# Kernel tuning notes

Measured on AMD Instinct MI355X. Metric: run time of the kernel, lower is better.

The kernel has to match this reference:

```python
import jax, jax.numpy as jnp
import numpy as np

V, N, K, D = 2, 100000, 8, 128
TAU = 1.0
LOG_2PI = float(np.log(2.0 * np.pi))


def setup_inputs() -> dict:
    key = jax.random.key(0)
    k1, k2, k3 = jax.random.split(key, 3)
    z = jax.random.normal(k1, (V, N, D), dtype=jnp.float32)
    phi = jnp.ones((V, K), dtype=jnp.float32) / K
    mu = jax.random.normal(k2, (V, K, D), dtype=jnp.float32)
    # sigma: identity (as in torch init) plus a small symmetric PSD perturbation
    a = 0.05 * jax.random.normal(k3, (V, K, D, D), dtype=jnp.float32)
    sigma = jnp.eye(D, dtype=jnp.float32) + jnp.einsum('vkde,vkfe->vkdf', a, a)
    return {"z": z, "phi": phi, "mu": mu, "sigma": sigma}


def _compute_energy(z, phi, mu, sigma):
    # z: [N, D]; phi: [K]; mu: [K, D]; sigma: [K, D, D]
    eps_eye = 1e-6 * jnp.eye(D, dtype=z.dtype)
    sigma_stable = sigma + eps_eye  # [K, D, D]
    inv_sigma = jnp.linalg.inv(sigma_stable)
    det_sigma = jnp.clip(jnp.linalg.det(sigma_stable), 1e-6, None)  # [K]
    diff = z[:, None, :] - mu[None, :, :]  # [N, K, D]
    maha = jnp.einsum('nkd,kde,nke->nk', diff, inv_sigma, diff)  # [N, K]
    log_pi = jax.nn.log_softmax(phi)  # [K]
    log_prob = (-0.5 * maha
                - 0.5 * D * LOG_2PI
                - 0.5 * jnp.log(det_sigma)[None, :]
                + log_pi[None, :])  # [N, K]
    energy = -jax.nn.logsumexp(log_prob, axis=1)  # [N]
    penalty = jnp.sum(1.0 / (jnp.diagonal(sigma_stable, axis1=-2, axis2=-1) + 1e-12))
    return energy, penalty


def reference(z, phi, mu, sigma):
    # vmap over views; energies_v: [V, N]
    energies_v, penalties = jax.vmap(_compute_energy)(z, phi, mu, sigma)
    energies = energies_v.T  # [N, V]
    total_energies = jnp.sum(energies)
    total_penalty = jnp.sum(penalties)
    weights = jax.nn.softmax(-energies / TAU, axis=1)  # [N, V]
    return energies, weights, total_energies, total_penalty
```

## Files before the change

### kernel.cpp

```cpp
#include <hip/hip_runtime.h>
#include <math.h>

#define V 2
#define NN 100000
#define KK 8
#define DD 128
#define TILE_N 128
#define SL 132
#define LOG2PI 1.8378770664093454f
#define LOG_1EM6 -13.815510557964274f

#define WLO_B 524288
#define BV_B  1048576
#define C_B   1056768

#define OUT_W_OFF (NN*V)
#define OUT_TE (2*NN*V)
#define OUT_TP (2*NN*V + 1)

typedef __attribute__((ext_vector_type(8))) short bf16x8;
typedef __attribute__((ext_vector_type(4))) float f32x4;

__device__ __forceinline__ unsigned short f2bf_rtn(float f) {
    unsigned u = __builtin_bit_cast(unsigned, f);
    unsigned r = u + 0x7FFFu + ((u >> 16) & 1u);
    return (unsigned short)(r >> 16);
}
__device__ __forceinline__ float bf2f(unsigned short h) {
    unsigned u = ((unsigned)h) << 16;
    return __builtin_bit_cast(float, u);
}

__global__ void zero_kernel(float* out) {
    int t = threadIdx.x;
    if (t < 2) out[OUT_TE + t] = 0.0f;
}

__global__ __launch_bounds__(256) void prep_kernel(const float* __restrict__ phi,
                                                   const float* __restrict__ mu,
                                                   const float* __restrict__ sigma,
                                                   void* __restrict__ wsv,
                                                   float* __restrict__ out) {
    __shared__ float Lf[DD * SL];
    __shared__ float Wcm[DD * SL];
    __shared__ float P[8][SL];
    __shared__ float dvec[DD];
    __shared__ float mulds[DD];
    __shared__ float red[256];
    __shared__ float Bv[8];

    const int tid = threadIdx.x;
    const int vk  = blockIdx.x;
    const int v   = vk >> 3;
    const int k   = vk & 7;
    const int R   = tid >> 4;
    const int C   = tid & 15;

    if (tid < DD) mulds[tid] = mu[vk * DD + tid];

    float A[8][8];
    const float* sig = sigma + (size_t)vk * DD * DD;
    float pen = 0.0f;
    #pragma unroll
    for (int a = 0; a < 8; ++a) {
        const float4* p4 = (const float4*)(sig + (size_t)(8 * R + a) * DD + 8 * C);
        float4 x = p4[0], y = p4[1];
        A[a][0] = x.x; A[a][1] = x.y; A[a][2] = x.z; A[a][3] = x.w;
        A[a][4] = y.x; A[a][5] = y.y; A[a][6] = y.z; A[a][7] = y.w;
        if (R == C) A[a][a] += 1e-6f;
    }
    if (R == C) {
        #pragma unroll
        for (int a = 0; a < 8; ++a) pen += 1.0f / (A[a][a] + 1e-12f);
    }

    for (int i = tid; i < DD * SL; i += 256) { Lf[i] = 0.0f; Wcm[i] = 0.0f; }

    red[tid] = pen;
    __syncthreads();
    for (int s = 128; s > 0; s >>= 1) {
        if (tid < s) red[tid] += red[tid + s];
        __syncthreads();
    }
    if (tid == 0) atomicAdd(&out[OUT_TP], red[0]);
    __syncthreads();

    for (int p = 0; p < 16; ++p) {
        if (C == p && R >= p) {
            #pragma unroll
            for (int b = 0; b < 8; ++b) {
                *(float4*)&P[b][8 * R]     = make_float4(A[0][b], A[1][b], A[2][b], A[3][b]);
                *(float4*)&P[b][8 * R + 4] = make_float4(A[4][b], A[5][b], A[6][b], A[7][b]);
            }
        }
        __syncthreads();

        if (tid < 64) {
            const int lane = tid;
            const int r1 = 8 * p + lane;
            const int r2 = r1 + 64;
            const bool ok2 = (r2 < DD);
            float pr1[8], pr2[8], rs[8];
            #pragma unroll
            for (int j = 0; j < 8; ++j) {
                pr1[j] = (r1 < DD) ? P[j][r1] : 0.0f;
                pr2[j] = ok2 ? P[j][r2] : 0.0f;
            }
            #pragma unroll
            for (int j = 0; j < 8; ++j) {
                if (lane >= j && lane < 8) Bv[lane] = pr1[j];
                __builtin_amdgcn_wave_barrier();
                float bv[8];
                #pragma unroll
                for (int m = 0; m < 8; ++m) bv[m] = Bv[m];
                __builtin_amdgcn_wave_barrier();
                float piv = bv[j];
                if (lane == j) dvec[8 * p + j] = piv;
                float inv2 = 1.0f / piv;
                rs[j] = rsqrtf(piv);
                float m1 = pr1[j] * inv2;
                float m2 = pr2[j] * inv2;
                #pragma unroll
                for (int j2 = 0; j2 < 8; ++j2) {
                    if (j2 > j) {
                        if (lane > j) pr1[j2] -= m1 * bv[j2];
                        pr2[j2] -= m2 * bv[j2];
                    }
                }
            }
            #pragma unroll
            for (int j = 0; j < 8; ++j) {
                if (r1 < DD) {
                    float v1 = (lane >= j) ? pr1[j] * rs[j] : 0.0f;
                    P[j][r1] = v1;
                    Lf[r1 * SL + 8 * p + j] = v1;
                }
                if (ok2) {
                    float v2 = pr2[j] * rs[j];
                    P[j][r2] = v2;
                    Lf[r2 * SL + 8 * p + j] = v2;
                }
            }
        }
        __syncthreads();

        if (C > p && R >= p) {
            #pragma unroll
            for (int j = 0; j < 8; ++j) {
                float4 a0 = *(const float4*)&P[j][8 * R];
                float4 a1 = *(const float4*)&P[j][8 * R + 4];
                float4 b0 = *(const float4*)&P[j][8 * C];
                float4 b1 = *(const float4*)&P[j][8 * C + 4];
                float ra[8] = {a0.x, a0.y, a0.z, a0.w, a1.x, a1.y, a1.z, a1.w};
                float rb[8] = {b0.x, b0.y, b0.z, b0.w, b1.x, b1.y, b1.z, b1.w};
                #pragma unroll
                for (int a = 0; a < 8; ++a)
                    #pragma unroll
                    for (int b = 0; b < 8; ++b)
                        A[a][b] -= ra[a] * rb[b];
            }
        }
        __syncthreads();
    }

    {
        const int j = tid >> 1;
        const int par = tid & 1;
        if (par == 0) Wcm[j * SL + j] = 1.0f / Lf[j * SL + j];
        __builtin_amdgcn_wave_barrier();
        const int pj0 = (j & ~3) + 4 * par;
        for (int i = j + 1; i < DD; ++i) {
            float s = 0.0f;
            for (int p4 = pj0; p4 < i; p4 += 8) {
                float4 lf = *(const float4*)&Lf[i * SL + p4];
                float4 wc = *(const float4*)&Wcm[j * SL + p4];
                s += lf.x * wc.x + lf.y * wc.y + lf.z * wc.z + lf.w * wc.w;
            }
            s += __shfl_xor(s, 1, 64);
            if (par == 0)
                Wcm[j * SL + i] = -s / Lf[i * SL + i];
        }
    }
    __syncthreads();

    if (tid < DD) {
        float b = 0.0f;
        for (int j2 = 0; j2 < DD; ++j2)
            b += Wcm[j2 * SL + tid] * mulds[j2];
        ((float*)((char*)wsv + BV_B))[vk * DD + tid] = b;
    }

    {
        unsigned* whi = (unsigned*)((unsigned short*)wsv + (size_t)vk * 16384);
        unsigned* wlo = (unsigned*)((unsigned short*)((char*)wsv + WLO_B) + (size_t)vk * 16384);
        const int r = tid >> 1;
        const int half = (tid & 1) * 64;
        for (int d0 = half; d0 < half + 64; d0 += 2) {
            float f0 = Wcm[d0 * SL + r];
            float f1 = Wcm[(d0 + 1) * SL + r];
            unsigned short h0 = f2bf_rtn(f0);
            unsigned short h1 = f2bf_rtn(f1);
            unsigned short l0 = f2bf_rtn(f0 - bf2f(h0));
            unsigned short l1 = f2bf_rtn(f1 - bf2f(h1));
            int g = d0 >> 3, e = d0 & 7;
            int idx = r * 128 + ((g ^ (r & 7)) << 3) + e;
            whi[idx >> 1] = (unsigned)h0 | ((unsigned)h1 << 16);
            wlo[idx >> 1] = (unsigned)l0 | ((unsigned)l1 << 16);
        }
    }

    red[tid] = (tid < DD) ? logf(dvec[tid]) : 0.0f;
    __syncthreads();
    for (int s = 128; s > 0; s >>= 1) {
        if (tid < s) red[tid] += red[tid + s];
        __syncthreads();
    }
    if (tid == 0) {
        float logdet_c = fmaxf(red[0], LOG_1EM6);
        const float* ph = phi + v * KK;
        float m = ph[0];
        for (int i = 1; i < KK; ++i) m = fmaxf(m, ph[i]);
        float s = 0.0f;
        for (int i = 0; i < KK; ++i) s += expf(ph[i] - m);
        float logpi = ph[k] - m - logf(s);
        ((float*)((char*)wsv + C_B))[vk] = logpi - 0.5f * logdet_c - 0.5f * (float)DD * LOG2PI;
    }
}

__global__ __launch_bounds__(256, 2) void energy_kernel(const float* __restrict__ z,
                                                        const void* __restrict__ wsv,
                                                        float* __restrict__ out) {
    __shared__ unsigned short wl[32768];
    __shared__ float maha_s[TILE_N][KK + 1];
    __shared__ float bl_s[DD];
    __shared__ float clds[V * KK];
    __shared__ float elds[TILE_N][V];
    __shared__ float red[256];

    const int tid  = threadIdx.x;
    const int lane = tid & 63;
    const int wave = tid >> 6;
    const int quad = lane >> 4;
    const int l16  = lane & 15;
    const int n0   = blockIdx.x * TILE_N;

    const unsigned short* whi_g = (const unsigned short*)wsv;
    const unsigned short* wlo_g = (const unsigned short*)((const char*)wsv + WLO_B);
    const float* b_g = (const float*)((const char*)wsv + BV_B);
    const float* c_g = (const float*)((const char*)wsv + C_B);

    if (tid < V * KK) clds[tid] = c_g[tid];

    float esum = 0.0f;

    for (int v = 0; v < V; ++v) {
        bf16x8 zhi[2][4], zlo[2][4];
        #pragma unroll
        for (int mt = 0; mt < 2; ++mt) {
            int n = n0 + wave * 32 + mt * 16 + l16;
            bool ok = (n < NN);
            const float* zp = z + ((size_t)v * NN + n) * DD + quad * 8;
            #pragma unroll
            for (int ds = 0; ds < 4; ++ds) {
                float f[8];
                if (ok) {
                    float4 a  = *(const float4*)(zp + ds * 32);
                    float4 bq = *(const float4*)(zp + ds * 32 + 4);
                    f[0] = a.x;  f[1] = a.y;  f[2] = a.z;  f[3] = a.w;
                    f[4] = bq.x; f[5] = bq.y; f[6] = bq.z; f[7] = bq.w;
                } else {
                    #pragma unroll
                    for (int e = 0; e < 8; ++e) f[e] = 0.0f;
                }
                bf16x8 hi8, lo8;
                #pragma unroll
                for (int e = 0; e < 8; ++e) {
                    unsigned short hu = f2bf_rtn(f[e]);
                    unsigned short lu = f2bf_rtn(f[e] - bf2f(hu));
                    hi8[e] = (short)hu;
                    lo8[e] = (short)lu;
                }
                zhi[mt][ds] = hi8;
                zlo[mt][ds] = lo8;
            }
        }

        for (int k = 0; k < KK; ++k) {
            const int vk = v * KK + k;
            __syncthreads();
            {
                const char* srch = (const char*)(whi_g + (size_t)vk * 16384);
                const char* srcl = (const char*)(wlo_g + (size_t)vk * 16384);
                char* ldsbase = (char*)wl;
                const int lane_off = wave * 1024 + lane * 16;
                #pragma unroll
                for (int t = 0; t < 8; ++t)
                    __builtin_amdgcn_global_load_lds(
                        (const __attribute__((address_space(1))) void*)(srch + t * 4096 + lane_off),
                        (__attribute__((address_space(3))) void*)(ldsbase + t * 4096 + wave * 1024),
                        16, 0, 0);
                #pragma unroll
                for (int t = 0; t < 8; ++t)
                    __builtin_amdgcn_global_load_lds(
                        (const __attribute__((address_space(1))) void*)(srcl + t * 4096 + lane_off),
                        (__attribute__((address_space(3))) void*)(ldsbase + 32768 + t * 4096 + wave * 1024),
                        16, 0, 0);
            }
            if (tid < DD) bl_s[tid] = b_g[vk * DD + tid];
            __syncthreads();

            f32x4 acc[2][8];
            #pragma unroll
            for (int mt = 0; mt < 2; ++mt)
                #pragma unroll
                for (int nt = 0; nt < 8; ++nt)
                    acc[mt][nt] = (f32x4)(0.0f);

            #pragma unroll
            for (int ds = 0; ds < 4; ++ds) {
                const int g = ds * 4 + quad;
                #pragma unroll
                for (int nt = 0; nt < 8; ++nt) {
                    if (nt < 2 * ds) continue;
                    int row = nt * 16 + l16;
                    int off = row * 128 + ((g ^ (row & 7)) << 3);
                    bf16x8 bh  = *(const bf16x8*)&wl[off];
                    bf16x8 blo = *(const bf16x8*)&wl[16384 + off];
                    #pragma unroll
                    for (int mt = 0; mt < 2; ++mt) {
                        acc[mt][nt] = __builtin_amdgcn_mfma_f32_16x16x32_bf16(zhi[mt][ds], bh,  acc[mt][nt], 0, 0, 0);
                        acc[mt][nt] = __builtin_amdgcn_mfma_f32_16x16x32_bf16(zhi[mt][ds], blo, acc[mt][nt], 0, 0, 0);
                        acc[mt][nt] = __builtin_amdgcn_mfma_f32_16x16x32_bf16(zlo[mt][ds], bh,  acc[mt][nt], 0, 0, 0);
                    }
                }
            }

            #pragma unroll
            for (int mt = 0; mt < 2; ++mt) {
                float p[4] = {0.f, 0.f, 0.f, 0.f};
                #pragma unroll
                for (int nt = 0; nt < 8; ++nt) {
                    float bc = bl_s[nt * 16 + l16];
                    f32x4 a = acc[mt][nt];
                    float y0 = a[0] - bc, y1 = a[1] - bc, y2 = a[2] - bc, y3 = a[3] - bc;
                    p[0] += y0 * y0; p[1] += y1 * y1; p[2] += y2 * y2; p[3] += y3 * y3;
                }
                #pragma unroll
                for (int reg = 0; reg < 4; ++reg) {
                    float s = p[reg];
                    s += __shfl_xor(s, 1, 64);
                    s += __shfl_xor(s, 2, 64);
                    s += __shfl_xor(s, 4, 64);
                    s += __shfl_xor(s, 8, 64);
                    if (l16 == 0)
                        maha_s[wave * 32 + mt * 16 + quad * 4 + reg][k] = s;
                }
            }
        }
        __syncthreads();

        if (tid < TILE_N && (n0 + tid) < NN) {
            float lp[KK];
            float m = -1e30f;
            #pragma unroll
            for (int k = 0; k < KK; ++k) {
                lp[k] = -0.5f * maha_s[tid][k] + clds[v * KK + k];
                m = fmaxf(m, lp[k]);
            }
            float s = 0.0f;
            #pragma unroll
            for (int k = 0; k < KK; ++k) s += expf(lp[k] - m);
            float e = -(m + logf(s));
            elds[tid][v] = e;
            esum += e;
        }
    }
    __syncthreads();

    if (tid < TILE_N && (n0 + tid) < NN) {
        int n = n0 + tid;
        float e0 = elds[tid][0];
        float e1 = elds[tid][1];
        float m = fmaxf(-e0, -e1);
        float x0 = expf(-e0 - m);
        float x1 = expf(-e1 - m);
        float inv = 1.0f / (x0 + x1);
        out[(size_t)n * V + 0] = e0;
        out[(size_t)n * V + 1] = e1;
        out[OUT_W_OFF + (size_t)n * V + 0] = x0 * inv;
        out[OUT_W_OFF + (size_t)n * V + 1] = x1 * inv;
    }

    red[tid] = esum;
    __syncthreads();
    for (int s = 128; s > 0; s >>= 1) {
        if (tid < s) red[tid] += red[tid + s];
        __syncthreads();
    }
    if (tid == 0) atomicAdd(&out[OUT_TE], red[0]);
}

extern "C" void kernel_launch(void* const* d_in, const int* in_sizes, int n_in,
                              void* d_out, int out_size, void* d_ws, size_t ws_size,
                              hipStream_t stream) {
    const float* z     = (const float*)d_in[0];
    const float* phi   = (const float*)d_in[1];
    const float* mu    = (const float*)d_in[2];
    const float* sigma = (const float*)d_in[3];
    float* out = (float*)d_out;

    hipLaunchKernelGGL(zero_kernel, dim3(1), dim3(64), 0, stream, out);
    hipLaunchKernelGGL(prep_kernel, dim3(V * KK), dim3(256), 0, stream, phi, mu, sigma, d_ws, out);
    int nblocks = (NN + TILE_N - 1) / TILE_N;
    hipLaunchKernelGGL(energy_kernel, dim3(nblocks), dim3(256), 0, stream, z, d_ws, out);
}
```

Baseline: 414.5 us.

## Double-buffer precomputed W images in LDS with padded layout and prefetch

Packs each component's hi/lo bf16 transformation matrix into one contiguous padded image (row stride 136) instead of XOR-swizzled separate hi/lo arrays. The energy kernel now double-buffers these images in LDS and prefetches the next component's image while computing the current one, using one barrier per iteration instead of two. All bias vectors are preloaded up front. LDS use grows to about 136KB per block and the launch bound drops the second block per CU, which lowers occupancy in exchange for overlapping loads with MFMA work.

```diff
diff --git a/kernel.cpp b/kernel.cpp
--- a/kernel.cpp
+++ b/kernel.cpp
@@ -10,9 +10,10 @@
 #define LOG2PI 1.8378770664093454f
 #define LOG_1EM6 -13.815510557964274f
 
-#define WLO_B 524288
-#define BV_B  1048576
-#define C_B   1056768
+#define IMG_B 69632
+#define IMG_HALF 17408
+#define BV_B  1114112
+#define C_B   1122304
 
 #define OUT_W_OFF (NN*V)
 #define OUT_TE (2*NN*V)
@@ -191,8 +192,7 @@
     }
 
     {
-        unsigned* whi = (unsigned*)((unsigned short*)wsv + (size_t)vk * 16384);
-        unsigned* wlo = (unsigned*)((unsigned short*)((char*)wsv + WLO_B) + (size_t)vk * 16384);
+        unsigned* Gp = (unsigned*)((char*)wsv + (size_t)vk * IMG_B);
         const int r = tid >> 1;
         const int half = (tid & 1) * 64;
         for (int d0 = half; d0 < half + 64; d0 += 2) {
@@ -202,10 +202,9 @@
             unsigned short h1 = f2bf_rtn(f1);
             unsigned short l0 = f2bf_rtn(f0 - bf2f(h0));
             unsigned short l1 = f2bf_rtn(f1 - bf2f(h1));
-            int g = d0 >> 3, e = d0 & 7;
-            int idx = r * 128 + ((g ^ (r & 7)) << 3) + e;
-            whi[idx >> 1] = (unsigned)h0 | ((unsigned)h1 << 16);
-            wlo[idx >> 1] = (unsigned)l0 | ((unsigned)l1 << 16);
+            int wi = (r * 136 + d0) >> 1;
+            Gp[wi] = (unsigned)h0 | ((unsigned)h1 << 16);
+            Gp[(IMG_HALF >> 1) + wi] = (unsigned)l0 | ((unsigned)l1 << 16);
         }
     }
 
@@ -227,14 +226,13 @@
     }
 }
 
-__global__ __launch_bounds__(256, 2) void energy_kernel(const float* __restrict__ z,
-                                                        const void* __restrict__ wsv,
-                                                        float* __restrict__ out) {
-    __shared__ unsigned short wl[32768];
-    __shared__ float maha_s[TILE_N][KK + 1];
-    __shared__ float bl_s[DD];
-    __shared__ float clds[V * KK];
-    __shared__ float elds[TILE_N][V];
+__global__ __launch_bounds__(256) void energy_kernel(const float* __restrict__ z,
+                                                     const void* __restrict__ wsv,
+                                                     float* __restrict__ out) {
+    __shared__ char wbuf[2 * IMG_B];
+    __shared__ float maha_s[V][TILE_N][KK + 1];
+    __shared__ float bl_all[16][DD];
+    __shared__ float clds[16];
     __shared__ float red[256];
 
     const int tid  = threadIdx.x;
@@ -244,143 +242,177 @@
     const int l16  = lane & 15;
     const int n0   = blockIdx.x * TILE_N;
 
-    const unsigned short* whi_g = (const unsigned short*)wsv;
-    const unsigned short* wlo_g = (const unsigned short*)((const char*)wsv + WLO_B);
     const float* b_g = (const float*)((const char*)wsv + BV_B);
     const float* c_g = (const float*)((const char*)wsv + C_B);
 
-    if (tid < V * KK) clds[tid] = c_g[tid];
+    for (int i = tid; i < 16 * DD; i += 256) ((float*)bl_all)[i] = b_g[i];
+    if (tid < 16) clds[tid] = c_g[tid];
+
+    const int lane_off = wave * 1024 + lane * 16;
+
+    {
+        const char* src = (const char*)wsv + 0 * IMG_B;
+        char* dst = wbuf;
+        #pragma unroll
+        for (int t = 0; t < 17; ++t)
+            __builtin_amdgcn_global_load_lds(
+                (const __attribute__((address_space(1))) void*)(src + t * 4096 + lane_off),
+                (__attribute__((address_space(3))) void*)(dst + t * 4096 + wave * 1024),
+                16, 0, 0);
+    }
+
+    bf16x8 zhi[2][4], zlo[2][4];
+    #pragma unroll
+    for (int mt = 0; mt < 2; ++mt) {
+        int n = n0 + wave * 32 + mt * 16 + l16;
+        bool ok = (n < NN);
+        const float* zp = z + ((size_t)0 * NN + n) * DD + quad * 8;
+        #pragma unroll
+        for (int ds = 0; ds < 4; ++ds) {
+            float f[8];
+            if (ok) {
+                float4 a  = *(const float4*)(zp + ds * 32);
+                float4 bq = *(const float4*)(zp + ds * 32 + 4);
+                f[0] = a.x;  f[1] = a.y;  f[2] = a.z;  f[3] = a.w;
+                f[4] = bq.x; f[5] = bq.y; f[6] = bq.z; f[7] = bq.w;
+            } else {
+                #pragma unroll
+                for (int e = 0; e < 8; ++e) f[e] = 0.0f;
+            }
+            bf16x8 hi8, lo8;
+            #pragma unroll
+            for (int e = 0; e < 8; ++e) {
+                unsigned short hu = f2bf_rtn(f[e]);
+                unsigned short lu = f2bf_rtn(f[e] - bf2f(hu));
+                hi8[e] = (short)hu;
+                lo8[e] = (short)lu;
+            }
+            zhi[mt][ds] = hi8;
+            zlo[mt][ds] = lo8;
+        }
+    }
+    __syncthreads();
+
+    for (int r = 0; r < 16; ++r) {
+        const int vv  = r >> 3;
+        const int k   = r & 7;
+        const int cur = r & 1;
+
+        if (r == 8) {
+            #pragma unroll
+            for (int mt = 0; mt < 2; ++mt) {
+                int n = n0 + wave * 32 + mt * 16 + l16;
+                bool ok = (n < NN);
+                const float* zp = z + ((size_t)1 * NN + n) * DD + quad * 8;
+                #pragma unroll
+                for (int ds = 0; ds < 4; ++ds) {
+                    float f[8];
+                    if (ok) {
+                        float4 a  = *(const float4*)(zp + ds * 32);
+                        float4 bq = *(const float4*)(zp + ds * 32 + 4);
+                        f[0] = a.x;  f[1] = a.y;  f[2] = a.z;  f[3] = a.w;
+                        f[4] = bq.x; f[5] = bq.y; f[6] = bq.z; f[7] = bq.w;
+                    } else {
+                        #pragma unroll
+                        for (int e = 0; e < 8; ++e) f[e] = 0.0f;
+                    }
+                    bf16x8 hi8, lo8;
+                    #pragma unroll
+                    for (int e = 0; e < 8; ++e) {
+                        unsigned short hu = f2bf_rtn(f[e]);
+                        unsigned short lu = f2bf_rtn(f[e] - bf2f(hu));
+                        hi8[e] = (short)hu;
+                        lo8[e] = (short)lu;
+                    }
+                    zhi[mt][ds] = hi8;
+                    zlo[mt][ds] = lo8;
+                }
+            }
+        }
+
+        if (r < 15) {
+            const char* src = (const char*)wsv + (size_t)(r + 1) * IMG_B;
+            char* dst = wbuf + (1 - cur) * IMG_B;
+            #pragma unroll
+            for (int t = 0; t < 17; ++t)
+                __builtin_amdgcn_global_load_lds(
+                    (const __attribute__((address_space(1))) void*)(src + t * 4096 + lane_off),
+                    (__attribute__((address_space(3))) void*)(dst + t * 4096 + wave * 1024),
+                    16, 0, 0);
+        }
+
+        const unsigned short* wb = (const unsigned short*)(wbuf + cur * IMG_B);
+
+        f32x4 acc[2][8];
+        #pragma unroll
+        for (int mt = 0; mt < 2; ++mt)
+            #pragma unroll
+            for (int nt = 0; nt < 8; ++nt)
+                acc[mt][nt] = (f32x4)(0.0f);
+
+        #pragma unroll
+        for (int ds = 0; ds < 4; ++ds) {
+            const int g = ds * 4 + quad;
+            #pragma unroll
+            for (int nt = 0; nt < 8; ++nt) {
+                if (nt < 2 * ds) continue;
+                int row = nt * 16 + l16;
+                int off = row * 136 + g * 8;
+                bf16x8 bh  = *(const bf16x8*)&wb[off];
+                bf16x8 blo = *(const bf16x8*)&wb[IMG_HALF + off];
+                #pragma unroll
+                for (int mt = 0; mt < 2; ++mt) {
+                    acc[mt][nt] = __builtin_amdgcn_mfma_f32_16x16x32_bf16(zhi[mt][ds], bh,  acc[mt][nt], 0, 0, 0);
+                    acc[mt][nt] = __builtin_amdgcn_mfma_f32_16x16x32_bf16(zhi[mt][ds], blo, acc[mt][nt], 0, 0, 0);
+                    acc[mt][nt] = __builtin_amdgcn_mfma_f32_16x16x32_bf16(zlo[mt][ds], bh,  acc[mt][nt], 0, 0, 0);
+                }
+            }
+        }
+
+        #pragma unroll
+        for (int mt = 0; mt < 2; ++mt) {
+            float p[4] = {0.f, 0.f, 0.f, 0.f};
+            #pragma unroll
+            for (int nt = 0; nt < 8; ++nt) {
+                float bc = bl_all[r][nt * 16 + l16];
+                f32x4 a = acc[mt][nt];
+                float y0 = a[0] - bc, y1 = a[1] - bc, y2 = a[2] - bc, y3 = a[3] - bc;
+                p[0] += y0 * y0; p[1] += y1 * y1; p[2] += y2 * y2; p[3] += y3 * y3;
+            }
+            #pragma unroll
+            for (int reg = 0; reg < 4; ++reg) {
+                float s = p[reg];
+                s += __shfl_xor(s, 1, 64);
+                s += __shfl_xor(s, 2, 64);
+                s += __shfl_xor(s, 4, 64);
+                s += __shfl_xor(s, 8, 64);
+                if (l16 == 0)
+                    maha_s[vv][wave * 32 + mt * 16 + quad * 4 + reg][k] = s;
+            }
+        }
+
+        __syncthreads();
+    }
 
     float esum = 0.0f;
-
-    for (int v = 0; v < V; ++v) {
-        bf16x8 zhi[2][4], zlo[2][4];
-        #pragma unroll
-        for (int mt = 0; mt < 2; ++mt) {
-            int n = n0 + wave * 32 + mt * 16 + l16;
-            bool ok = (n < NN);
-            const float* zp = z + ((size_t)v * NN + n) * DD + quad * 8;
-            #pragma unroll
-            for (int ds = 0; ds < 4; ++ds) {
-                float f[8];
-                if (ok) {
-                    float4 a  = *(const float4*)(zp + ds * 32);
-                    float4 bq = *(const float4*)(zp + ds * 32 + 4);
-                    f[0] = a.x;  f[1] = a.y;  f[2] = a.z;  f[3] = a.w;
-                    f[4] = bq.x; f[5] = bq.y; f[6] = bq.z; f[7] = bq.w;
-                } else {
-                    #pragma unroll
-                    for (int e = 0; e < 8; ++e) f[e] = 0.0f;
-                }
-                bf16x8 hi8, lo8;
-                #pragma unroll
-                for (int e = 0; e < 8; ++e) {
-                    unsigned short hu = f2bf_rtn(f[e]);
-                    unsigned short lu = f2bf_rtn(f[e] - bf2f(hu));
-                    hi8[e] = (short)hu;
-                    lo8[e] = (short)lu;
-                }
-                zhi[mt][ds] = hi8;
-                zlo[mt][ds] = lo8;
-            }
-        }
-
-        for (int k = 0; k < KK; ++k) {
-            const int vk = v * KK + k;
-            __syncthreads();
-            {
-                const char* srch = (const char*)(whi_g + (size_t)vk * 16384);
-                const char* srcl = (const char*)(wlo_g + (size_t)vk * 16384);
-                char* ldsbase = (char*)wl;
-                const int lane_off = wave * 1024 + lane * 16;
-                #pragma unroll
-                for (int t = 0; t < 8; ++t)
-                    __builtin_amdgcn_global_load_lds(
-                        (const __attribute__((address_space(1))) void*)(srch + t * 4096 + lane_off),
-                        (__attribute__((address_space(3))) void*)(ldsbase + t * 4096 + wave * 1024),
-                        16, 0, 0);
-                #pragma unroll
-                for (int t = 0; t < 8; ++t)
-                    __builtin_amdgcn_global_load_lds(
-                        (const __attribute__((address_space(1))) void*)(srcl + t * 4096 + lane_off),
-                        (__attribute__((address_space(3))) void*)(ldsbase + 32768 + t * 4096 + wave * 1024),
-                        16, 0, 0);
-            }
-            if (tid < DD) bl_s[tid] = b_g[vk * DD + tid];
-            __syncthreads();
-
-            f32x4 acc[2][8];
-            #pragma unroll
-            for (int mt = 0; mt < 2; ++mt)
-                #pragma unroll
-                for (int nt = 0; nt < 8; ++nt)
-                    acc[mt][nt] = (f32x4)(0.0f);
-
-            #pragma unroll
-            for (int ds = 0; ds < 4; ++ds) {
-                const int g = ds * 4 + quad;
-                #pragma unroll
-                for (int nt = 0; nt < 8; ++nt) {
-                    if (nt < 2 * ds) continue;
-                    int row = nt * 16 + l16;
-                    int off = row * 128 + ((g ^ (row & 7)) << 3);
-                    bf16x8 bh  = *(const bf16x8*)&wl[off];
-                    bf16x8 blo = *(const bf16x8*)&wl[16384 + off];
-                    #pragma unroll
-                    for (int mt = 0; mt < 2; ++mt) {
-                        acc[mt][nt] = __builtin_amdgcn_mfma_f32_16x16x32_bf16(zhi[mt][ds], bh,  acc[mt][nt], 0, 0, 0);
-                        acc[mt][nt] = __builtin_amdgcn_mfma_f32_16x16x32_bf16(zhi[mt][ds], blo, acc[mt][nt], 0, 0, 0);
-                        acc[mt][nt] = __builtin_amdgcn_mfma_f32_16x16x32_bf16(zlo[mt][ds], bh,  acc[mt][nt], 0, 0, 0);
-                    }
-                }
-            }
-
-            #pragma unroll
-            for (int mt = 0; mt < 2; ++mt) {
-                float p[4] = {0.f, 0.f, 0.f, 0.f};
-                #pragma unroll
-                for (int nt = 0; nt < 8; ++nt) {
-                    float bc = bl_s[nt * 16 + l16];
-                    f32x4 a = acc[mt][nt];
-                    float y0 = a[0] - bc, y1 = a[1] - bc, y2 = a[2] - bc, y3 = a[3] - bc;
-                    p[0] += y0 * y0; p[1] += y1 * y1; p[2] += y2 * y2; p[3] += y3 * y3;
-                }
-                #pragma unroll
-                for (int reg = 0; reg < 4; ++reg) {
-                    float s = p[reg];
-                    s += __shfl_xor(s, 1, 64);
-                    s += __shfl_xor(s, 2, 64);
-                    s += __shfl_xor(s, 4, 64);
-                    s += __shfl_xor(s, 8, 64);
-                    if (l16 == 0)
-                        maha_s[wave * 32 + mt * 16 + quad * 4 + reg][k] = s;
-                }
-            }
-        }
-        __syncthreads();
-
-        if (tid < TILE_N && (n0 + tid) < NN) {
+    if (tid < TILE_N && (n0 + tid) < NN) {
+        float ev[V];
+        #pragma unroll
+        for (int vv = 0; vv < V; ++vv) {
             float lp[KK];
             float m = -1e30f;
             #pragma unroll
             for (int k = 0; k < KK; ++k) {
-                lp[k] = -0.5f * maha_s[tid][k] + clds[v * KK + k];
+                lp[k] = -0.5f * maha_s[vv][tid][k] + clds[vv * KK + k];
                 m = fmaxf(m, lp[k]);
             }
             float s = 0.0f;
             #pragma unroll
             for (int k = 0; k < KK; ++k) s += expf(lp[k] - m);
-            float e = -(m + logf(s));
-            elds[tid][v] = e;
-            esum += e;
-        }
-    }
-    __syncthreads();
-
-    if (tid < TILE_N && (n0 + tid) < NN) {
+            ev[vv] = -(m + logf(s));
+        }
         int n = n0 + tid;
-        float e0 = elds[tid][0];
-        float e1 = elds[tid][1];
+        float e0 = ev[0], e1 = ev[1];
         float m = fmaxf(-e0, -e1);
         float x0 = expf(-e0 - m);
         float x1 = expf(-e1 - m);
@@ -389,6 +421,7 @@
         out[(size_t)n * V + 1] = e1;
         out[OUT_W_OFF + (size_t)n * V + 0] = x0 * inv;
         out[OUT_W_OFF + (size_t)n * V + 1] = x1 * inv;
+        esum = e0 + e1;
     }
 
     red[tid] = esum;
```

Result: slower. 512.1 us (+23.5%).

## Split prep into Cholesky and parallel TRSM, restructure maha over (chunk, component) grid

Applied to the files above, without the earlier changes.

The single prep kernel is split in two. The first factorises each covariance and computes the mean-solve vector by forward substitution. The second inverts the triangular factor using four blocks per component, spreading that serial work across 64 blocks instead of 16. The energy kernel becomes a maha kernel on a 2D grid over point chunks and the 16 view-component pairs: each block loads its inverse-factor image into LDS once and reuses it across 8 tiles, instead of reloading it per component per tile. The per-component Mahalanobis values go to a workspace buffer, and a separate finalize kernel does the logsumexp and softmax. This adds global traffic for that buffer and extra launches, and z is now read 8 times per view.

```diff
diff --git a/kernel.cpp b/kernel.cpp
--- a/kernel.cpp
+++ b/kernel.cpp
@@ -7,12 +7,19 @@
 #define DD 128
 #define TILE_N 128
 #define SL 132
+#define NT 782
+#define CH 8
+#define NCHUNK 98
+#define NPAD 100096
 #define LOG2PI 1.8378770664093454f
 #define LOG_1EM6 -13.815510557964274f
 
-#define WLO_B 524288
-#define BV_B  1048576
-#define C_B   1056768
+#define IMG_B 69632
+#define IMG_HALF 17408
+#define LF_B   1114112
+#define BV_B   2228224
+#define C_B    2236416
+#define MAHA_B 2236480
 
 #define OUT_W_OFF (NN*V)
 #define OUT_TE (2*NN*V)
@@ -36,18 +43,18 @@
     if (t < 2) out[OUT_TE + t] = 0.0f;
 }
 
-__global__ __launch_bounds__(256) void prep_kernel(const float* __restrict__ phi,
-                                                   const float* __restrict__ mu,
-                                                   const float* __restrict__ sigma,
-                                                   void* __restrict__ wsv,
-                                                   float* __restrict__ out) {
+__global__ __launch_bounds__(256) void prep_chol(const float* __restrict__ phi,
+                                                 const float* __restrict__ mu,
+                                                 const float* __restrict__ sigma,
+                                                 void* __restrict__ wsv,
+                                                 float* __restrict__ out) {
     __shared__ float Lf[DD * SL];
-    __shared__ float Wcm[DD * SL];
     __shared__ float P[8][SL];
     __shared__ float dvec[DD];
     __shared__ float mulds[DD];
     __shared__ float red[256];
     __shared__ float Bv[8];
+    __shared__ float Bb[DD];
 
     const int tid = threadIdx.x;
     const int vk  = blockIdx.x;
@@ -74,7 +81,7 @@
         for (int a = 0; a < 8; ++a) pen += 1.0f / (A[a][a] + 1e-12f);
     }
 
-    for (int i = tid; i < DD * SL; i += 256) { Lf[i] = 0.0f; Wcm[i] = 0.0f; }
+    for (int i = tid; i < DD * SL; i += 256) Lf[i] = 0.0f;
 
     red[tid] = pen;
     __syncthreads();
@@ -163,50 +170,27 @@
         __syncthreads();
     }
 
+    if (tid < 64) {
+        const int lane = tid;
+        float acc0 = mulds[lane];
+        float acc1 = mulds[lane + 64];
+        for (int j = 0; j < DD; ++j) {
+            if (j < 64) { if (lane == j)      Bb[j] = acc0 / Lf[j * SL + j]; }
+            else        { if (lane == j - 64) Bb[j] = acc1 / Lf[j * SL + j]; }
+            __builtin_amdgcn_wave_barrier();
+            float bj = Bb[j];
+            __builtin_amdgcn_wave_barrier();
+            if (lane > j)      acc0 -= Lf[lane * SL + j] * bj;
+            if (lane + 64 > j) acc1 -= Lf[(lane + 64) * SL + j] * bj;
+        }
+    }
+    __syncthreads();
+    if (tid < DD) ((float*)((char*)wsv + BV_B))[vk * DD + tid] = Bb[tid];
+
     {
-        const int j = tid >> 1;
-        const int par = tid & 1;
-        if (par == 0) Wcm[j * SL + j] = 1.0f / Lf[j * SL + j];
-        __builtin_amdgcn_wave_barrier();
-        const int pj0 = (j & ~3) + 4 * par;
-        for (int i = j + 1; i < DD; ++i) {
-            float s = 0.0f;
-            for (int p4 = pj0; p4 < i; p4 += 8) {
-                float4 lf = *(const float4*)&Lf[i * SL + p4];
-                float4 wc = *(const float4*)&Wcm[j * SL + p4];
-                s += lf.x * wc.x + lf.y * wc.y + lf.z * wc.z + lf.w * wc.w;
-            }
-            s += __shfl_xor(s, 1, 64);
-            if (par == 0)
-                Wcm[j * SL + i] = -s / Lf[i * SL + i];
-        }
-    }
-    __syncthreads();
-
-    if (tid < DD) {
-        float b = 0.0f;
-        for (int j2 = 0; j2 < DD; ++j2)
-            b += Wcm[j2 * SL + tid] * mulds[j2];
-        ((float*)((char*)wsv + BV_B))[vk * DD + tid] = b;
-    }
-
-    {
-        unsigned* whi = (unsigned*)((unsigned short*)wsv + (size_t)vk * 16384);
-        unsigned* wlo = (unsigned*)((unsigned short*)((char*)wsv + WLO_B) + (size_t)vk * 16384);
-        const int r = tid >> 1;
-        const int half = (tid & 1) * 64;
-        for (int d0 = half; d0 < half + 64; d0 += 2) {
-            float f0 = Wcm[d0 * SL + r];
-            float f1 = Wcm[(d0 + 1) * SL + r];
-            unsigned short h0 = f2bf_rtn(f0);
-            unsigned short h1 = f2bf_rtn(f1);
-            unsigned short l0 = f2bf_rtn(f0 - bf2f(h0));
-            unsigned short l1 = f2bf_rtn(f1 - bf2f(h1));
-            int g = d0 >> 3, e = d0 & 7;
-            int idx = r * 128 + ((g ^ (r & 7)) << 3) + e;
-            whi[idx >> 1] = (unsigned)h0 | ((unsigned)h1 << 16);
-            wlo[idx >> 1] = (unsigned)l0 | ((unsigned)l1 << 16);
-        }
+        float4* Lg = (float4*)((char*)wsv + LF_B + (size_t)vk * IMG_B);
+        const float4* Ls4 = (const float4*)Lf;
+        for (int i = tid; i < DD * SL / 4; i += 256) Lg[i] = Ls4[i];
     }
 
     red[tid] = (tid < DD) ? logf(dvec[tid]) : 0.0f;
@@ -227,39 +211,95 @@
     }
 }
 
-__global__ __launch_bounds__(256, 2) void energy_kernel(const float* __restrict__ z,
-                                                        const void* __restrict__ wsv,
-                                                        float* __restrict__ out) {
-    __shared__ unsigned short wl[32768];
-    __shared__ float maha_s[TILE_N][KK + 1];
+__global__ __launch_bounds__(256) void prep_trsm(void* __restrict__ wsv) {
+    __shared__ float Ls[DD * SL];
+    __shared__ float Wc[32][SL];
+
+    const int tid = threadIdx.x;
+    const int vk  = blockIdx.x >> 2;
+    const int cg  = blockIdx.x & 3;
+
+    const float4* Lg = (const float4*)((const char*)wsv + LF_B + (size_t)vk * IMG_B);
+    float4* Ls4 = (float4*)Ls;
+    for (int i = tid; i < DD * SL / 4; i += 256) Ls4[i] = Lg[i];
+    __syncthreads();
+
+    const int c   = tid >> 3;
+    const int par = tid & 7;
+    const int j   = 4 * c + cg;
+
+    for (int e = par; e < SL; e += 8) Wc[c][e] = 0.0f;
+    if (par == 0) Wc[c][j] = 1.0f / Ls[j * SL + j];
+    __builtin_amdgcn_wave_barrier();
+
+    const int pbase = j & ~3;
+    for (int i = j + 1; i < DD; ++i) {
+        float s = 0.0f;
+        for (int p4 = pbase + 4 * par; p4 < i; p4 += 32) {
+            float4 lf = *(const float4*)&Ls[i * SL + p4];
+            float4 wc = *(const float4*)&Wc[c][p4];
+            s += lf.x * wc.x + lf.y * wc.y + lf.z * wc.z + lf.w * wc.w;
+        }
+        s += __shfl_xor(s, 1, 64);
+        s += __shfl_xor(s, 2, 64);
+        s += __shfl_xor(s, 4, 64);
+        if (par == 0) Wc[c][i] = -s / Ls[i * SL + i];
+        __builtin_amdgcn_wave_barrier();
+    }
+
+    unsigned short* Gh = (unsigned short*)((char*)wsv + (size_t)vk * IMG_B);
+    unsigned short* Gl = Gh + IMG_HALF;
+    for (int i2 = par; i2 < DD; i2 += 8) {
+        float f = (i2 >= j) ? Wc[c][i2] : 0.0f;
+        unsigned short h = f2bf_rtn(f);
+        unsigned short l = f2bf_rtn(f - bf2f(h));
+        Gh[i2 * 136 + j] = h;
+        Gl[i2 * 136 + j] = l;
+    }
+}
+
+__global__ __launch_bounds__(256, 2) void maha_kernel(const float* __restrict__ z,
+                                                      void* __restrict__ wsv) {
+    __shared__ unsigned short wl[IMG_B / 2];
     __shared__ float bl_s[DD];
-    __shared__ float clds[V * KK];
-    __shared__ float elds[TILE_N][V];
-    __shared__ float red[256];
 
     const int tid  = threadIdx.x;
     const int lane = tid & 63;
     const int wave = tid >> 6;
     const int quad = lane >> 4;
     const int l16  = lane & 15;
-    const int n0   = blockIdx.x * TILE_N;
-
-    const unsigned short* whi_g = (const unsigned short*)wsv;
-    const unsigned short* wlo_g = (const unsigned short*)((const char*)wsv + WLO_B);
-    const float* b_g = (const float*)((const char*)wsv + BV_B);
-    const float* c_g = (const float*)((const char*)wsv + C_B);
-
-    if (tid < V * KK) clds[tid] = c_g[tid];
-
-    float esum = 0.0f;
-
-    for (int v = 0; v < V; ++v) {
+    const int r     = blockIdx.y;
+    const int chunk = blockIdx.x;
+    const int vv    = r >> 3;
+
+    {
+        const char* src = (const char*)wsv + (size_t)r * IMG_B;
+        char* dst = (char*)wl;
+        const int lane_off = wave * 1024 + lane * 16;
+        #pragma unroll
+        for (int t = 0; t < 17; ++t)
+            __builtin_amdgcn_global_load_lds(
+                (const __attribute__((address_space(1))) void*)(src + t * 4096 + lane_off),
+                (__attribute__((address_space(3))) void*)(dst + t * 4096 + wave * 1024),
+                16, 0, 0);
+    }
+    if (tid < DD) bl_s[tid] = ((const float*)((const char*)wsv + BV_B))[r * DD + tid];
+    __syncthreads();
+
+    const float* zbase = z + (size_t)vv * NN * DD;
+    float* mrow = (float*)((char*)wsv + MAHA_B) + (size_t)r * NPAD;
+
+    for (int ti = 0; ti < CH; ++ti) {
+        const int t = chunk * CH + ti;
+        if (t >= NT) break;
+        const int n0 = t * TILE_N;
+
         bf16x8 zhi[2][4], zlo[2][4];
         #pragma unroll
         for (int mt = 0; mt < 2; ++mt) {
             int n = n0 + wave * 32 + mt * 16 + l16;
             bool ok = (n < NN);
-            const float* zp = z + ((size_t)v * NN + n) * DD + quad * 8;
+            const float* zp = zbase + (size_t)n * DD + quad * 8;
             #pragma unroll
             for (int ds = 0; ds < 4; ++ds) {
                 float f[8];
@@ -285,102 +325,90 @@
             }
         }
 
-        for (int k = 0; k < KK; ++k) {
-            const int vk = v * KK + k;
-            __syncthreads();
-            {
-                const char* srch = (const char*)(whi_g + (size_t)vk * 16384);
-                const char* srcl = (const char*)(wlo_g + (size_t)vk * 16384);
-                char* ldsbase = (char*)wl;
-                const int lane_off = wave * 1024 + lane * 16;
+        f32x4 acc[2][8];
+        #pragma unroll
+        for (int mt = 0; mt < 2; ++mt)
+            #pragma unroll
+            for (int nt = 0; nt < 8; ++nt)
+                acc[mt][nt] = (f32x4)(0.0f);
+
+        #pragma unroll
+        for (int ds = 0; ds < 4; ++ds) {
+            const int g = ds * 4 + quad;
+            #pragma unroll
+            for (int nt = 0; nt < 8; ++nt) {
+                if (nt < 2 * ds) continue;
+                int row = nt * 16 + l16;
+                int off = row * 136 + g * 8;
+                bf16x8 bh  = *(const bf16x8*)&wl[off];
+                bf16x8 blo = *(const bf16x8*)&wl[IMG_HALF + off];
                 #pragma unroll
-                for (int t = 0; t < 8; ++t)
-                    __builtin_amdgcn_global_load_lds(
-                        (const __attribute__((address_space(1))) void*)(srch + t * 4096 + lane_off),
-                        (__attribute__((address_space(3))) void*)(ldsbase + t * 4096 + wave * 1024),
-                        16, 0, 0);
-                #pragma unroll
-                for (int t = 0; t < 8; ++t)
-                    __builtin_amdgcn_global_load_lds(
-                        (const __attribute__((address_space(1))) void*)(srcl + t * 4096 + lane_off),
-                        (__attribute__((address_space(3))) void*)(ldsbase + 32768 + t * 4096 + wave * 1024),
-                        16, 0, 0);
-            }
-            if (tid < DD) bl_s[tid] = b_g[vk * DD + tid];
-            __syncthreads();
-
-            f32x4 acc[2][8];
-            #pragma unroll
-            for (int mt = 0; mt < 2; ++mt)
-                #pragma unroll
-                for (int nt = 0; nt < 8; ++nt)
-                    acc[mt][nt] = (f32x4)(0.0f);
-
-            #pragma unroll
-            for (int ds = 0; ds < 4; ++ds) {
-                const int g = ds * 4 + quad;
-                #pragma unroll
-                for (int nt = 0; nt < 8; ++nt) {
-                    if (nt < 2 * ds) continue;
-                    int row = nt * 16 + l16;
-                    int off = row * 128 + ((g ^ (row & 7)) << 3);
-                    bf16x8 bh  = *(const bf16x8*)&wl[off];
-                    bf16x8 blo = *(const bf16x8*)&wl[16384 + off];
-                    #pragma unroll
-                    for (int mt = 0; mt < 2; ++mt) {
-                        acc[mt][nt] = __builtin_amdgcn_mfma_f32_16x16x32_bf16(zhi[mt][ds], bh,  acc[mt][nt], 0, 0, 0);
-                        acc[mt][nt] = __builtin_amdgcn_mfma_f32_16x16x32_bf16(zhi[mt][ds], blo, acc[mt][nt], 0, 0, 0);
-                        acc[mt][nt] = __builtin_amdgcn_mfma_f32_16x16x32_bf16(zlo[mt][ds], bh,  acc[mt][nt], 0, 0, 0);
-                    }
-                }
-            }
-
-            #pragma unroll
-            for (int mt = 0; mt < 2; ++mt) {
-                float p[4] = {0.f, 0.f, 0.f, 0.f};
-                #pragma unroll
-                for (int nt = 0; nt < 8; ++nt) {
-                    float bc = bl_s[nt * 16 + l16];
-                    f32x4 a = acc[mt][nt];
-                    float y0 = a[0] - bc, y1 = a[1] - bc, y2 = a[2] - bc, y3 = a[3] - bc;
-                    p[0] += y0 * y0; p[1] += y1 * y1; p[2] += y2 * y2; p[3] += y3 * y3;
-                }
-                #pragma unroll
-                for (int reg = 0; reg < 4; ++reg) {
-                    float s = p[reg];
-                    s += __shfl_xor(s, 1, 64);
-                    s += __shfl_xor(s, 2, 64);
-                    s += __shfl_xor(s, 4, 64);
-                    s += __shfl_xor(s, 8, 64);
-                    if (l16 == 0)
-                        maha_s[wave * 32 + mt * 16 + quad * 4 + reg][k] = s;
-                }
-            }
-        }
-        __syncthreads();
-
-        if (tid < TILE_N && (n0 + tid) < NN) {
+                for (int mt = 0; mt < 2; ++mt) {
+                    acc[mt][nt] = __builtin_amdgcn_mfma_f32_16x16x32_bf16(zhi[mt][ds], bh,  acc[mt][nt], 0, 0, 0);
+                    acc[mt][nt] = __builtin_amdgcn_mfma_f32_16x16x32_bf16(zhi[mt][ds], blo, acc[mt][nt], 0, 0, 0);
+                    acc[mt][nt] = __builtin_amdgcn_mfma_f32_16x16x32_bf16(zlo[mt][ds], bh,  acc[mt][nt], 0, 0, 0);
+                }
+            }
+        }
+
+        #pragma unroll
+        for (int mt = 0; mt < 2; ++mt) {
+            float p[4] = {0.f, 0.f, 0.f, 0.f};
+            #pragma unroll
+            for (int nt = 0; nt < 8; ++nt) {
+                float bc = bl_s[nt * 16 + l16];
+                f32x4 a = acc[mt][nt];
+                float y0 = a[0] - bc, y1 = a[1] - bc, y2 = a[2] - bc, y3 = a[3] - bc;
+                p[0] += y0 * y0; p[1] += y1 * y1; p[2] += y2 * y2; p[3] += y3 * y3;
+            }
+            float sv[4];
+            #pragma unroll
+            for (int reg = 0; reg < 4; ++reg) {
+                float s = p[reg];
+                s += __shfl_xor(s, 1, 64);
+                s += __shfl_xor(s, 2, 64);
+                s += __shfl_xor(s, 4, 64);
+                s += __shfl_xor(s, 8, 64);
+                sv[reg] = s;
+            }
+            if (l16 == 0)
+                *(float4*)&mrow[n0 + wave * 32 + mt * 16 + quad * 4] =
+                    make_float4(sv[0], sv[1], sv[2], sv[3]);
+        }
+    }
+}
+
+__global__ __launch_bounds__(256) void finalize_kernel(const void* __restrict__ wsv,
+                                                       float* __restrict__ out) {
+    __shared__ float red[256];
+    __shared__ float clds[16];
+
+    const int tid = threadIdx.x;
+    if (tid < 16) clds[tid] = ((const float*)((const char*)wsv + C_B))[tid];
+    __syncthreads();
+
+    const float* mahap = (const float*)((const char*)wsv + MAHA_B);
+    const int n = blockIdx.x * 256 + tid;
+    float esum = 0.0f;
+
+    if (n < NN) {
+        float ev[V];
+        #pragma unroll
+        for (int vv = 0; vv < V; ++vv) {
             float lp[KK];
             float m = -1e30f;
             #pragma unroll
             for (int k = 0; k < KK; ++k) {
-                lp[k] = -0.5f * maha_s[tid][k] + clds[v * KK + k];
+                int r = vv * KK + k;
+                lp[k] = -0.5f * mahap[(size_t)r * NPAD + n] + clds[r];
                 m = fmaxf(m, lp[k]);
             }
             float s = 0.0f;
             #pragma unroll
             for (int k = 0; k < KK; ++k) s += expf(lp[k] - m);
-            float e = -(m + logf(s));
-            elds[tid][v] = e;
-            esum += e;
-        }
-    }
-    __syncthreads();
-
-    if (tid < TILE_N && (n0 + tid) < NN) {
-        int n = n0 + tid;
-        float e0 = elds[tid][0];
-        float e1 = elds[tid][1];
+            ev[vv] = -(m + logf(s));
+        }
+        float e0 = ev[0], e1 = ev[1];
         float m = fmaxf(-e0, -e1);
         float x0 = expf(-e0 - m);
         float x1 = expf(-e1 - m);
@@ -389,6 +417,7 @@
         out[(size_t)n * V + 1] = e1;
         out[OUT_W_OFF + (size_t)n * V + 0] = x0 * inv;
         out[OUT_W_OFF + (size_t)n * V + 1] = x1 * inv;
+        esum = e0 + e1;
     }
 
     red[tid] = esum;
@@ -410,7 +439,8 @@
     float* out = (float*)d_out;
 
     hipLaunchKernelGGL(zero_kernel, dim3(1), dim3(64), 0, stream, out);
-    hipLaunchKernelGGL(prep_kernel, dim3(V * KK), dim3(256), 0, stream, phi, mu, sigma, d_ws, out);
-    int nblocks = (NN + TILE_N - 1) / TILE_N;
-    hipLaunchKernelGGL(energy_kernel, dim3(nblocks), dim3(256), 0, stream, z, d_ws, out);
-}
+    hipLaunchKernelGGL(prep_chol, dim3(V * KK), dim3(256), 0, stream, phi, mu, sigma, d_ws, out);
+    hipLaunchKernelGGL(prep_trsm, dim3(64), dim3(256), 0, stream, d_ws);
+    hipLaunchKernelGGL(maha_kernel, dim3(NCHUNK, 16), dim3(256), 0, stream, z, d_ws);
+    hipLaunchKernelGGL(finalize_kernel, dim3((NPAD + 255) / 256), dim3(256), 0, stream, d_ws, out);
+}
```

Result: faster. 400.5 us (-3.4%).
